# Optimization experiments

Hardware: AMD Instinct MI355X
Metric: run time of the kernel (lower is better)

Reference implementation:

```python
import jax, jax.numpy as jnp
import numpy as np


def setup_inputs() -> dict:
    key = jax.random.key(0)
    k1, k2 = jax.random.split(key)
    N, C, H, W = 4, 64, 128, 256
    x = jax.random.normal(k1, (N, C, H, W), dtype=jnp.float32)
    y = jax.random.normal(k2, (N, C, H, W), dtype=jnp.float32)
    return {"x": x, "y": y, "maxdisp": 48}


def reference(x, y, maxdisp):
    # corr[n, i, h, w] = sum_c x[n,c,h,w] * y[n,c,h,w-i]  (zero where w-i < 0)
    # Matches the torch loop: y is left-padded by maxdisp-1 zeros, and output
    # channel i (loop d = maxdisp-1-i, reversed) takes slice d : d+W of y_pad.
    D = int(maxdisp)
    N, C, H, W = x.shape
    y_pad = jnp.pad(y, ((0, 0), (0, 0), (0, 0), (D - 1, 0)))  # [N,C,H,W+D-1]
    corr_slices = []
    for i in range(D):  # fixed small disparity set, not a data dim
        y_slice = jax.lax.slice_in_dim(y_pad, D - 1 - i, D - 1 - i + W, axis=3)
        corr_slices.append(jnp.einsum('nchw,nchw->nhw', x, y_slice))
    corr = jnp.stack(corr_slices, axis=1)  # [N,D,H,W]
    return corr
```

## Files before the change

### kernel.cpp

```cpp
#include <hip/hip_runtime.h>

#define N_ 4
#define C_ 64
#define H_ 128
#define W_ 256
#define D_ 48
#define ROWS (W_ + D_)

__global__ __launch_bounds__(256, 2)
void corr1d_kernel(const float* __restrict__ x,
                   const float* __restrict__ y,
                   float* __restrict__ out) {
    __shared__ float ysh[C_][ROWS];

    const int t  = threadIdx.x;
    const int nh = blockIdx.x;
    const int n  = nh / H_;
    const int h  = nh % H_;

    const size_t in_base = ((size_t)n * C_ * H_ + h) * W_;

    #pragma unroll
    for (int k = 0; k < (C_ * D_) / 256; ++k) {
        int idx = k * 256 + t;
        int c = idx / D_;
        int j = idx % D_;
        ysh[c][j] = 0.0f;
    }

    #pragma unroll
    for (int k = 0; k < (C_ * W_ / 4) / 256; ++k) {
        int idx = k * 256 + t;
        int c = idx / (W_ / 4);
        int q = idx % (W_ / 4);
        const float4 v = *reinterpret_cast<const float4*>(
            &y[in_base + (size_t)c * (H_ * W_) + q * 4]);
        *reinterpret_cast<float4*>(&ysh[c][D_ + q * 4]) = v;
    }

    __syncthreads();

    float acc[D_];
    #pragma unroll
    for (int i = 0; i < D_; ++i) acc[i] = 0.0f;

    const int w = t;

    for (int c = 0; c < C_; ++c) {
        const float xv = x[in_base + (size_t)c * (H_ * W_) + w];
        const float* yrow = &ysh[c][w];
        #pragma unroll
        for (int i = 0; i < D_; ++i) {
            acc[i] += xv * yrow[D_ - i];
        }
    }

    const size_t out_base = ((size_t)n * D_ * H_ + h) * W_ + w;
    #pragma unroll
    for (int i = 0; i < D_; ++i) {
        out[out_base + (size_t)i * (H_ * W_)] = acc[i];
    }
}

extern "C" void kernel_launch(void* const* d_in, const int* in_sizes, int n_in,
                              void* d_out, int out_size, void* d_ws, size_t ws_size,
                              hipStream_t stream) {
    (void)in_sizes; (void)n_in; (void)out_size; (void)d_ws; (void)ws_size;
    const float* x = (const float*)d_in[0];
    const float* y = (const float*)d_in[1];
    float* out = (float*)d_out;

    dim3 grid(N_ * H_);
    dim3 block(256);
    corr1d_kernel<<<grid, block, 0, stream>>>(x, y, out);
}
```

Baseline: 123.2 us.

## Register-tile correlation over 4 widths x 12 disparities with channel-chunked LDS staging

Replaces the one-thread-per-column, 48-disparity kernel with a register-blocked scheme. Each thread computes a 4-wide by 12-disparity tile from float4 LDS reads, and x is staged in shared memory alongside y. Channels are processed in chunks of 16 so LDS use shrinks, and the grid splits W into two 128-wide tiles for twice as many blocks. Outputs are written as float4, which raises arithmetic intensity per LDS load but adds halo reloads and per-chunk barriers.

```diff
diff --git a/kernel.cpp b/kernel.cpp
--- a/kernel.cpp
+++ b/kernel.cpp
@@ -5,60 +5,105 @@
 #define H_ 128
 #define W_ 256
 #define D_ 48
-#define ROWS (W_ + D_)
+#define HW_ (H_ * W_)
 
-__global__ __launch_bounds__(256, 2)
-void corr1d_kernel(const float* __restrict__ x,
-                   const float* __restrict__ y,
-                   float* __restrict__ out) {
-    __shared__ float ysh[C_][ROWS];
+#define WTILE 128
+#define HALO  D_
+#define YCOLS (WTILE + HALO)
+#define CCHUNK 16
+#define NCHUNK (C_ / CCHUNK)
+#define VT 4
+#define DT 12
+#define NIG (D_ / DT)
+#define NTW (WTILE / VT)
+#define NTHREADS (NTW * NIG)
+
+__global__ __launch_bounds__(NTHREADS, 2)
+void corr1d_v2(const float* __restrict__ x,
+               const float* __restrict__ y,
+               float* __restrict__ out) {
+    __shared__ __align__(16) float ysh[CCHUNK][YCOLS];
+    __shared__ __align__(16) float xsh[CCHUNK][WTILE];
 
     const int t  = threadIdx.x;
-    const int nh = blockIdx.x;
+    const int tw = t & (NTW - 1);
+    const int ig = t >> 5;
+    const int b  = blockIdx.x;
+    const int wt = (b & 1) * WTILE;
+    const int nh = b >> 1;
     const int n  = nh / H_;
     const int h  = nh % H_;
 
     const size_t in_base = ((size_t)n * C_ * H_ + h) * W_;
 
+    const int i0 = ig * DT;
+    const int w0 = wt + tw * VT;
+
+    float acc[DT][VT];
     #pragma unroll
-    for (int k = 0; k < (C_ * D_) / 256; ++k) {
-        int idx = k * 256 + t;
-        int c = idx / D_;
-        int j = idx % D_;
-        ysh[c][j] = 0.0f;
+    for (int k = 0; k < DT; ++k)
+        #pragma unroll
+        for (int v = 0; v < VT; ++v) acc[k][v] = 0.f;
+
+    const int js = 4 * tw - DT * ig + (HALO - DT + 1) - 1;
+
+    for (int ch = 0; ch < NCHUNK; ++ch) {
+        const int c0 = ch * CCHUNK;
+
+        #pragma unroll
+        for (int kk = 0; kk < 6; ++kk) {
+            int idx = kk * NTHREADS + t;
+            if (idx < CCHUNK * (YCOLS / 4)) {
+                int r = idx / (YCOLS / 4);
+                int q = idx % (YCOLS / 4);
+                int w = wt - HALO + 4 * q;
+                float4 v;
+                if (w >= 0)
+                    v = *reinterpret_cast<const float4*>(
+                        &y[in_base + (size_t)(c0 + r) * HW_ + w]);
+                else
+                    v = make_float4(0.f, 0.f, 0.f, 0.f);
+                *reinterpret_cast<float4*>(&ysh[r][4 * q]) = v;
+            }
+        }
+        #pragma unroll
+        for (int kk = 0; kk < 4; ++kk) {
+            int idx = kk * NTHREADS + t;
+            int r = idx / (WTILE / 4);
+            int q = idx % (WTILE / 4);
+            float4 v = *reinterpret_cast<const float4*>(
+                &x[in_base + (size_t)(c0 + r) * HW_ + wt + 4 * q]);
+            *reinterpret_cast<float4*>(&xsh[r][4 * q]) = v;
+        }
+        __syncthreads();
+
+        #pragma unroll 4
+        for (int cc = 0; cc < CCHUNK; ++cc) {
+            const float4 q0 = *reinterpret_cast<const float4*>(&ysh[cc][js]);
+            const float4 q1 = *reinterpret_cast<const float4*>(&ysh[cc][js + 4]);
+            const float4 q2 = *reinterpret_cast<const float4*>(&ysh[cc][js + 8]);
+            const float4 q3 = *reinterpret_cast<const float4*>(&ysh[cc][js + 12]);
+            const float4 xq = *reinterpret_cast<const float4*>(&xsh[cc][tw * VT]);
+            const float r_[16] = {q0.x, q0.y, q0.z, q0.w,
+                                  q1.x, q1.y, q1.z, q1.w,
+                                  q2.x, q2.y, q2.z, q2.w,
+                                  q3.x, q3.y, q3.z, q3.w};
+            const float xv[VT] = {xq.x, xq.y, xq.z, xq.w};
+            #pragma unroll
+            for (int k = 0; k < DT; ++k)
+                #pragma unroll
+                for (int v = 0; v < VT; ++v)
+                    acc[k][v] = fmaf(xv[v], r_[12 + v - k], acc[k][v]);
+        }
+        __syncthreads();
     }
 
+    const size_t ob = ((size_t)(n * D_ + i0) * H_ + h) * W_ + w0;
     #pragma unroll
-    for (int k = 0; k < (C_ * W_ / 4) / 256; ++k) {
-        int idx = k * 256 + t;
-        int c = idx / (W_ / 4);
-        int q = idx % (W_ / 4);
-        const float4 v = *reinterpret_cast<const float4*>(
-            &y[in_base + (size_t)c * (H_ * W_) + q * 4]);
-        *reinterpret_cast<float4*>(&ysh[c][D_ + q * 4]) = v;
-    }
-
-    __syncthreads();
-
-    float acc[D_];
-    #pragma unroll
-    for (int i = 0; i < D_; ++i) acc[i] = 0.0f;
-
-    const int w = t;
-
-    for (int c = 0; c < C_; ++c) {
-        const float xv = x[in_base + (size_t)c * (H_ * W_) + w];
-        const float* yrow = &ysh[c][w];
-        #pragma unroll
-        for (int i = 0; i < D_; ++i) {
-            acc[i] += xv * yrow[D_ - i];
-        }
-    }
-
-    const size_t out_base = ((size_t)n * D_ * H_ + h) * W_ + w;
-    #pragma unroll
-    for (int i = 0; i < D_; ++i) {
-        out[out_base + (size_t)i * (H_ * W_)] = acc[i];
+    for (int k = 0; k < DT; ++k) {
+        float4 o;
+        o.x = acc[k][0]; o.y = acc[k][1]; o.z = acc[k][2]; o.w = acc[k][3];
+        *reinterpret_cast<float4*>(&out[ob + (size_t)k * HW_]) = o;
     }
 }
 
@@ -70,7 +115,7 @@
     const float* y = (const float*)d_in[1];
     float* out = (float*)d_out;
 
-    dim3 grid(N_ * H_);
-    dim3 block(256);
-    corr1d_kernel<<<grid, block, 0, stream>>>(x, y, out);
+    dim3 grid(N_ * H_ * (W_ / WTILE));
+    dim3 block(NTHREADS);
+    corr1d_v2<<<grid, block, 0, stream>>>(x, y, out);
 }
```

Result: faster. 117.7 us (-4.5%).
